# Kernel optimization log

Hardware: AMD Instinct MI355X
Metric: run time of the kernel (lower is better)

## Reference

```python
import jax, jax.numpy as jnp
import numpy as np

N_NODES, N_EDGES = 100000, 800000
F_NODE, F_EDGE, N_CLASSES = 128, 16, 10


def _lin(key, fan_in, fan_out, bias=True):
    k1, k2 = jax.random.split(key)
    W = jax.random.normal(k1, (fan_in, fan_out), jnp.float32) * 0.05
    if bias:
        b = jax.random.normal(k2, (fan_out,), jnp.float32) * 0.05
        return W, b
    return (W,)


def setup_inputs() -> dict:
    key = jax.random.key(0)
    ks = jax.random.split(key, 24)
    inp = {
        "x": jax.random.normal(ks[0], (N_NODES, F_NODE), jnp.float32),
        "edge_index": jax.random.randint(ks[1], (2, N_EDGES), 0, N_NODES, jnp.int64 if jax.config.jax_enable_x64 else jnp.int32),
        "edge_attr": jax.random.normal(ks[2], (N_EDGES, F_EDGE), jnp.float32),
    }
    dims = [(F_NODE, 128), (128, 128), (128, 256)]  # (in_channels, out_channels) per layer
    i = 3
    for li, (din, dout) in enumerate(dims, start=1):
        inp[f"Wq{li}"], inp[f"bq{li}"] = _lin(ks[i], din, dout); i += 1
        inp[f"Wk{li}"], inp[f"bk{li}"] = _lin(ks[i], din, dout); i += 1
        inp[f"Wv{li}"], inp[f"bv{li}"] = _lin(ks[i], din, dout); i += 1
        (inp[f"We{li}"],) = _lin(ks[i], F_EDGE, dout, bias=False); i += 1  # PyG lin_edge: bias=False
        inp[f"Ws{li}"], inp[f"bs{li}"] = _lin(ks[i], din, dout); i += 1  # root/skip weight
    inp["Wc"], inp["bc"] = _lin(ks[i], 256, N_CLASSES)
    return inp


def transformer_conv(x, src, dst, edge_attr, Wq, bq, Wk, bk, Wv, bv, We, Ws, bs):
    """PyG TransformerConv, heads=1, concat=True, root_weight=True."""
    N = x.shape[0]
    C = Wq.shape[1]
    q = x @ Wq + bq                      # [N, C]
    k = x @ Wk + bk                      # [N, C]
    v = x @ Wv + bv                      # [N, C]
    e = edge_attr @ We                   # [E, C] edge-conditioned term
    # per-edge attention logits: <q_i, k_j + e_ij> / sqrt(C)
    alpha = jnp.sum(q[dst] * (k[src] + e), axis=-1) / jnp.sqrt(jnp.float32(C))  # [E]
    # segment softmax over edges sharing a destination node
    m = jax.ops.segment_max(alpha, dst, num_segments=N)
    p = jnp.exp(alpha - m[dst])
    s = jax.ops.segment_sum(p, dst, num_segments=N)
    a = p / (s[dst] + 1e-16)
    # scatter-aggregate weighted messages (value_j + edge term)
    out = jax.ops.segment_sum(a[:, None] * (v[src] + e), dst, num_segments=N)  # [N, C]
    return out + x @ Ws + bs             # root/skip connection


def reference(x, edge_index, edge_attr,
              Wq1, bq1, Wk1, bk1, Wv1, bv1, We1, Ws1, bs1,
              Wq2, bq2, Wk2, bk2, Wv2, bv2, We2, Ws2, bs2,
              Wq3, bq3, Wk3, bk3, Wv3, bv3, We3, Ws3, bs3,
              Wc, bc):
    src, dst = edge_index[0], edge_index[1]
    h = transformer_conv(x, src, dst, edge_attr, Wq1, bq1, Wk1, bk1, Wv1, bv1, We1, Ws1, bs1)
    h = jax.nn.relu(h)  # dropout is identity in eval mode
    h = transformer_conv(h, src, dst, edge_attr, Wq2, bq2, Wk2, bk2, Wv2, bv2, We2, Ws2, bs2)
    h = jax.nn.relu(h)
    h = transformer_conv(h, src, dst, edge_attr, Wq3, bq3, Wk3, bk3, Wv3, bv3, We3, Ws3, bs3)
    return h @ Wc + bc                   # [N, num_classes]
```

## Files before the change

kernel.cpp:

```cpp
#include <hip/hip_runtime.h>
#include <math.h>


typedef unsigned int uint;
typedef unsigned short ushort;
typedef _Float16 f16x8 __attribute__((ext_vector_type(8)));
typedef _Float16 h16x2 __attribute__((ext_vector_type(2)));
typedef float f32x4 __attribute__((ext_vector_type(4)));
typedef float f32x2 __attribute__((ext_vector_type(2)));

__device__ __forceinline__ ushort f2h(float f) {
    return __builtin_bit_cast(ushort, (_Float16)f);
}
__device__ __forceinline__ float h2f(ushort h) {
    return (float)__builtin_bit_cast(_Float16, h);
}
__device__ __forceinline__ h16x2 bch2(uint u) { return __builtin_bit_cast(h16x2, u); }
__device__ __forceinline__ f32x2 cvt2(uint u) {
    h16x2 h = bch2(u);
    return (f32x2){(float)h.x, (float)h.y};
}

#if __has_builtin(__builtin_amdgcn_fdot2)
#define FDOT2(a, b, c) __builtin_amdgcn_fdot2((a), (b), (c), false)
#else
__device__ __forceinline__ float fdot2_sw(h16x2 a, h16x2 b, float c) {
    return fmaf((float)a.x, (float)b.x, fmaf((float)a.y, (float)b.y, c));
}
#define FDOT2(a, b, c) fdot2_sw((a), (b), (c))
#endif

__global__ void k_zero(uint* p, int n) {
    int i = blockIdx.x * 256 + threadIdx.x;
    if (i < n) p[i] = 0u;
}

__global__ void k_hist(const int* __restrict__ dst, uint* __restrict__ counts, int E, int N) {
    int e = blockIdx.x * 256 + threadIdx.x;
    if (e < E) {
        int d = dst[e];
        d = (d < 0) ? 0 : (d >= N ? N - 1 : d);
        atomicAdd(&counts[d], 1u);
    }
}

__global__ void k_scan1(const uint* __restrict__ counts, uint* __restrict__ bsum, int n) {
    __shared__ uint sm[256];
    int tid = threadIdx.x;
    int base = blockIdx.x * 1024 + tid * 4;
    uint s = 0;
#pragma unroll
    for (int j = 0; j < 4; ++j)
        if (base + j < n) s += counts[base + j];
    sm[tid] = s;
    __syncthreads();
    for (int d = 128; d > 0; d >>= 1) {
        if (tid < d) sm[tid] += sm[tid + d];
        __syncthreads();
    }
    if (tid == 0) bsum[blockIdx.x] = sm[0];
}

__global__ void k_scan2(uint* bsum, int nb) {
    if (threadIdx.x == 0 && blockIdx.x == 0) {
        uint run = 0;
        for (int i = 0; i < nb; ++i) { uint v = bsum[i]; bsum[i] = run; run += v; }
    }
}

__global__ void k_scan3(const uint* __restrict__ counts, const uint* __restrict__ bsum,
                        uint* __restrict__ row_ptr, int n, int E) {
    __shared__ uint sm[256];
    int tid = threadIdx.x;
    int base = blockIdx.x * 1024 + tid * 4;
    uint local[4];
    uint s = 0;
#pragma unroll
    for (int j = 0; j < 4; ++j) {
        local[j] = (base + j < n) ? counts[base + j] : 0u;
        s += local[j];
    }
    sm[tid] = s;
    __syncthreads();
    for (int d = 1; d < 256; d <<= 1) {
        uint v = (tid >= d) ? sm[tid - d] : 0u;
        __syncthreads();
        sm[tid] += v;
        __syncthreads();
    }
    uint run = sm[tid] - s + bsum[blockIdx.x];
#pragma unroll
    for (int j = 0; j < 4; ++j)
        if (base + j < n) { row_ptr[base + j] = run; run += local[j]; }
    if (blockIdx.x == 0 && tid == 0) row_ptr[n] = (uint)E;
}

__global__ void k_fill(const int* __restrict__ ei, const uint* __restrict__ row_ptr,
                       uint* __restrict__ cursor, int2* __restrict__ srcid, int E, int N) {
    int e = blockIdx.x * 256 + threadIdx.x;
    if (e >= E) return;
    int s = ei[e];
    int d = ei[E + e];
    s = (s < 0) ? 0 : (s >= N ? N - 1 : s);
    d = (d < 0) ? 0 : (d >= N ? N - 1 : d);
    uint idx = row_ptr[d] + atomicAdd(&cursor[d], 1u);
    srcid[idx] = make_int2(s, e);
}

__global__ void k_cvt(const float4* __restrict__ in, ushort4* __restrict__ outp, int n4) {
    int i = blockIdx.x * 256 + threadIdx.x;
    if (i >= n4) return;
    float4 v = in[i];
    ushort4 o;
    o.x = f2h(v.x); o.y = f2h(v.y); o.z = f2h(v.z); o.w = f2h(v.w);
    outp[i] = o;
}

__global__ void k_packg(const float* __restrict__ Wq, const float* __restrict__ bq,
                        const float* __restrict__ We, float* __restrict__ Wgf,
                        float* __restrict__ bgf, int C) {
    int id = blockIdx.x * 256 + threadIdx.x;
    if (id < 2048) {
        int k = id >> 4, f = id & 15;
        float s = 0.f;
        for (int c = 0; c < C; ++c) s = fmaf(Wq[k * C + c], We[f * C + c], s);
        Wgf[id] = s;
    } else if (id < 2064) {
        int f = id - 2048;
        float s = 0.f;
        for (int c = 0; c < C; ++c) s = fmaf(bq[c], We[f * C + c], s);
        bgf[f] = s;
    }
}

__global__ void k_packw(const float* __restrict__ Wq, const float* __restrict__ Wk,
                        const float* __restrict__ Wv, const float* __restrict__ Ws,
                        const float* __restrict__ Wgf, ushort* __restrict__ Bp, int C) {
    int nct = (4 * C + 16) >> 4;
    int total = 4 * nct * 512;
    int id = blockIdx.x * 256 + threadIdx.x;
    if (id >= total) return;
    int j = id & 7;
    int rest = id >> 3;
    int lane = rest & 63;
    rest >>= 6;
    int ct = rest % nct;
    int kt = rest / nct;
    int k = kt * 32 + ((lane >> 4) << 3) + j;
    int c = (ct << 4) + (lane & 15);
    float w;
    if (c < 4 * C) {
        int mat = c / C, cc = c % C;
        const float* W = (mat == 0) ? Wq : (mat == 1) ? Wk : (mat == 2) ? Wv : Ws;
        w = W[k * C + cc];
    } else {
        w = Wgf[k * 16 + (c - 4 * C)];
    }
    Bp[id] = f2h(w);
}

__global__ void k_bias(const float* __restrict__ bq, const float* __restrict__ bk,
                       const float* __restrict__ bv, const float* __restrict__ bs,
                       const float* __restrict__ bgf, float* __restrict__ outp, int C) {
    int c = blockIdx.x * 256 + threadIdx.x;
    if (c >= 4 * C + 16) return;
    float v;
    if (c < 4 * C) {
        int mat = c / C, cc = c % C;
        const float* b = (mat == 0) ? bq : (mat == 1) ? bk : (mat == 2) ? bv : bs;
        v = b[cc];
    } else {
        v = bgf[c - 4 * C];
    }
    outp[c] = v;
}

__global__ __launch_bounds__(256, 4) void k_gemm(const ushort* __restrict__ A,
                                                 const ushort* __restrict__ Bp,
                                                 const float* __restrict__ bias,
                                                 ushort* __restrict__ H,
                                                 ushort* __restrict__ S,
                                                 ushort* __restrict__ g,
                                                 int C, int mt_total) {
    constexpr int RT = 8;
    int fourC = 4 * C, threeC = 3 * C;
    int P = fourC + 16;
    int nct = P >> 4;
    int lane = threadIdx.x & 63;
    int wave = threadIdx.x >> 6;
    int quad = lane >> 4;
    int r = lane & 15;
    int c0 = (blockIdx.x << 8) + (wave << 6);
    int ct0 = c0 >> 4;
    if (ct0 >= nct) return;

    f16x8 bf[16];
#pragma unroll
    for (int kk = 0; kk < 4; ++kk)
#pragma unroll
        for (int i = 0; i < 4; ++i) {
            if (ct0 + i < nct)
                bf[kk * 4 + i] = *(const f16x8*)(Bp + ((size_t)((kk * nct + ct0 + i) << 6) + lane) * 8);
            else
                bf[kk * 4 + i] = __builtin_bit_cast(f16x8, (uint4){0u, 0u, 0u, 0u});
        }

    float bi4[4];
#pragma unroll
    for (int i = 0; i < 4; ++i) {
        int cc = c0 + (i << 4) + r;
        bi4[i] = (cc < P) ? bias[cc] : 0.f;
    }

    int mt0 = blockIdx.y * RT;
    int mt_end = mt0 + RT;
    if (mt_end > mt_total) mt_end = mt_total;

    for (int mt = mt0; mt < mt_end; ++mt) {
        int m0 = mt << 4;
        const ushort* arow = A + (size_t)(m0 + r) * 128 + (quad << 3);

        f32x4 acc[4];
#pragma unroll
        for (int i = 0; i < 4; ++i) acc[i] = (f32x4){0.f, 0.f, 0.f, 0.f};

#pragma unroll
        for (int kk = 0; kk < 4; ++kk) {
            f16x8 a = *(const f16x8*)(arow + kk * 32);
#pragma unroll
            for (int i = 0; i < 4; ++i)
                if (ct0 + i < nct)
                    acc[i] = __builtin_amdgcn_mfma_f32_16x16x32_f16(a, bf[kk * 4 + i], acc[i], 0, 0, 0);
        }

#pragma unroll
        for (int i = 0; i < 4; ++i) {
            int cc = c0 + (i << 4) + r;
            if (cc >= P) continue;
#pragma unroll
            for (int reg = 0; reg < 4; ++reg) {
                int rr = m0 + (quad << 2) + reg;
                ushort val = f2h(acc[i][reg] + bi4[i]);
                if (cc < threeC)      H[(size_t)rr * threeC + cc] = val;
                else if (cc < fourC)  S[(size_t)rr * C + (cc - threeC)] = val;
                else                  g[(size_t)rr * 16 + (cc - fourC)] = val;
            }
        }
    }
}

template <int C, int GSIZE>
__global__ __launch_bounds__(256, 6) void k_edge1(const ushort* __restrict__ H,
                                                  ushort* g,
                                                  const uint* __restrict__ row_ptr,
                                                  const int2* __restrict__ srcid,
                                                  const float* __restrict__ eattr,
                                                  ushort* __restrict__ ebuf,
                                                  float* __restrict__ lbuf, int N) {
    constexpr int VR = C / GSIZE;
    constexpr int TH = 3 * C;
    constexpr int GPB = 256 / GSIZE;
    const float scale = (C == 128) ? 0.08838834764831843f : 0.0625f;
    const float foldk = 16.0f / (float)GSIZE;

    int lane = threadIdx.x & (GSIZE - 1);
    int grp = threadIdx.x / GSIZE;
    int f = lane & 15;
    int node = blockIdx.x * GPB + grp;
    if (node >= N) return;
    int lvr = lane * VR;

    uint4 qv = *(const uint4*)(H + (size_t)node * TH + lvr);
    h16x2 q0 = bch2(qv.x), q1 = bch2(qv.y), q2 = bch2(qv.z), q3 = bch2(qv.w);
    float fg = foldk * h2f(g[(size_t)node * 16 + f]);
    uint beg = row_ptr[node], end = row_ptr[node + 1];

    float l = 0.f, w = 0.f;
    for (uint t = beg; t < end; t += 4) {
        uint t1 = (t + 1 < end) ? t + 1 : t;
        uint t2 = (t + 2 < end) ? t + 2 : t;
        uint t3 = (t + 3 < end) ? t + 3 : t;
        int2 se0 = srcid[t], se1 = srcid[t1], se2 = srcid[t2], se3 = srcid[t3];
        float at0 = eattr[(size_t)se0.y * 16 + f];
        float at1 = eattr[(size_t)se1.y * 16 + f];
        float at2 = eattr[(size_t)se2.y * 16 + f];
        float at3 = eattr[(size_t)se3.y * 16 + f];
        uint4 k0 = *(const uint4*)(H + (size_t)se0.x * TH + C + lvr);
        uint4 k1 = *(const uint4*)(H + (size_t)se1.x * TH + C + lvr);
        uint4 k2 = *(const uint4*)(H + (size_t)se2.x * TH + C + lvr);
        uint4 k3 = *(const uint4*)(H + (size_t)se3.x * TH + C + lvr);

        float p0 = at0 * fg, p1 = at1 * fg, p2 = at2 * fg, p3 = at3 * fg;
        p0 = FDOT2(q0, bch2(k0.x), p0); p0 = FDOT2(q1, bch2(k0.y), p0);
        p0 = FDOT2(q2, bch2(k0.z), p0); p0 = FDOT2(q3, bch2(k0.w), p0);
        p1 = FDOT2(q0, bch2(k1.x), p1); p1 = FDOT2(q1, bch2(k1.y), p1);
        p1 = FDOT2(q2, bch2(k1.z), p1); p1 = FDOT2(q3, bch2(k1.w), p1);
        p2 = FDOT2(q0, bch2(k2.x), p2); p2 = FDOT2(q1, bch2(k2.y), p2);
        p2 = FDOT2(q2, bch2(k2.z), p2); p2 = FDOT2(q3, bch2(k2.w), p2);
        p3 = FDOT2(q0, bch2(k3.x), p3); p3 = FDOT2(q1, bch2(k3.y), p3);
        p3 = FDOT2(q2, bch2(k3.z), p3); p3 = FDOT2(q3, bch2(k3.w), p3);

        p0 += __shfl_xor(p0, 1); p1 += __shfl_xor(p1, 1);
        p2 += __shfl_xor(p2, 1); p3 += __shfl_xor(p3, 1);
        p0 += __shfl_xor(p0, 2); p1 += __shfl_xor(p1, 2);
        p2 += __shfl_xor(p2, 2); p3 += __shfl_xor(p3, 2);
        p0 += __shfl_xor(p0, 4); p1 += __shfl_xor(p1, 4);
        p2 += __shfl_xor(p2, 4); p3 += __shfl_xor(p3, 4);
        p0 += __shfl_xor(p0, 8); p1 += __shfl_xor(p1, 8);
        p2 += __shfl_xor(p2, 8); p3 += __shfl_xor(p3, 8);
        if (GSIZE == 32) {
            p0 += __shfl_xor(p0, 16); p1 += __shfl_xor(p1, 16);
            p2 += __shfl_xor(p2, 16); p3 += __shfl_xor(p3, 16);
        }
        float e0 = __expf(p0 * scale);
        float e1 = (t + 1 < end) ? __expf(p1 * scale) : 0.f;
        float e2 = (t + 2 < end) ? __expf(p2 * scale) : 0.f;
        float e3 = (t + 3 < end) ? __expf(p3 * scale) : 0.f;
        l += (e0 + e1) + (e2 + e3);
        w = fmaf(e0, at0, w); w = fmaf(e1, at1, w);
        w = fmaf(e2, at2, w); w = fmaf(e3, at3, w);
        if (lane < 4) {
            uint tj = t + lane;
            if (tj < end) {
                float ee = (lane == 0) ? e0 : (lane == 1) ? e1 : (lane == 2) ? e2 : e3;
                ebuf[tj] = f2h(ee);
            }
        }
    }
    if (lane < 16) g[(size_t)node * 16 + lane] = f2h(w);
    if (lane == 0) lbuf[node] = l;
}

template <int C, int GSIZE, bool RELU>
__global__ __launch_bounds__(256, 6) void k_edge2(const ushort* __restrict__ H,
                                                  ushort* __restrict__ S,
                                                  const uint* __restrict__ row_ptr,
                                                  const int2* __restrict__ srcid,
                                                  const ushort* __restrict__ ebuf,
                                                  const ushort* __restrict__ wbuf,
                                                  const float* __restrict__ lbuf,
                                                  const float* __restrict__ We, int N) {
    constexpr int VR = C / GSIZE;
    constexpr int TH = 3 * C;
    constexpr int GPB = 256 / GSIZE;
    __shared__ float swex[GPB][17];

    int lane = threadIdx.x & (GSIZE - 1);
    int grp = threadIdx.x / GSIZE;
    int node = blockIdx.x * GPB + grp;
    if (node >= N) return;
    int lvr = lane * VR;
    uint beg = row_ptr[node], end = row_ptr[node + 1];

    ushort* srow = S + (size_t)node * C + lvr;
    uint4 skv = *(const uint4*)srow;
    if (lane < 16) swex[grp][lane] = h2f(wbuf[(size_t)node * 16 + lane]);
    float l = lbuf[node];

    f32x2 acc[4];
#pragma unroll
    for (int j = 0; j < 4; ++j) acc[j] = (f32x2){0.f, 0.f};

    for (uint t = beg; t < end; t += 4) {
        uint t1 = (t + 1 < end) ? t + 1 : t;
        uint t2 = (t + 2 < end) ? t + 2 : t;
        uint t3 = (t + 3 < end) ? t + 3 : t;
        int s0 = srcid[t].x, s1 = srcid[t1].x, s2 = srcid[t2].x, s3 = srcid[t3].x;
        float e0 = h2f(ebuf[t]);
        float e1 = (t + 1 < end) ? h2f(ebuf[t1]) : 0.f;
        float e2 = (t + 2 < end) ? h2f(ebuf[t2]) : 0.f;
        float e3 = (t + 3 < end) ? h2f(ebuf[t3]) : 0.f;
        uint4 v0 = *(const uint4*)(H + (size_t)s0 * TH + 2 * C + lvr);
        uint4 v1 = *(const uint4*)(H + (size_t)s1 * TH + 2 * C + lvr);
        uint4 v2 = *(const uint4*)(H + (size_t)s2 * TH + 2 * C + lvr);
        uint4 v3 = *(const uint4*)(H + (size_t)s3 * TH + 2 * C + lvr);
        f32x2 eb;
        eb = (f32x2){e0, e0};
        acc[0] = __builtin_elementwise_fma(cvt2(v0.x), eb, acc[0]);
        acc[1] = __builtin_elementwise_fma(cvt2(v0.y), eb, acc[1]);
        acc[2] = __builtin_elementwise_fma(cvt2(v0.z), eb, acc[2]);
        acc[3] = __builtin_elementwise_fma(cvt2(v0.w), eb, acc[3]);
        eb = (f32x2){e1, e1};
        acc[0] = __builtin_elementwise_fma(cvt2(v1.x), eb, acc[0]);
        acc[1] = __builtin_elementwise_fma(cvt2(v1.y), eb, acc[1]);
        acc[2] = __builtin_elementwise_fma(cvt2(v1.z), eb, acc[2]);
        acc[3] = __builtin_elementwise_fma(cvt2(v1.w), eb, acc[3]);
        eb = (f32x2){e2, e2};
        acc[0] = __builtin_elementwise_fma(cvt2(v2.x), eb, acc[0]);
        acc[1] = __builtin_elementwise_fma(cvt2(v2.y), eb, acc[1]);
        acc[2] = __builtin_elementwise_fma(cvt2(v2.z), eb, acc[2]);
        acc[3] = __builtin_elementwise_fma(cvt2(v2.w), eb, acc[3]);
        eb = (f32x2){e3, e3};
        acc[0] = __builtin_elementwise_fma(cvt2(v3.x), eb, acc[0]);
        acc[1] = __builtin_elementwise_fma(cvt2(v3.y), eb, acc[1]);
        acc[2] = __builtin_elementwise_fma(cvt2(v3.z), eb, acc[2]);
        acc[3] = __builtin_elementwise_fma(cvt2(v3.w), eb, acc[3]);
    }

    float inv = 1.f / (l + 1e-16f);
    f32x2 ew[4];
#pragma unroll
    for (int j = 0; j < 4; ++j) ew[j] = (f32x2){0.f, 0.f};
#pragma unroll
    for (int f2i = 0; f2i < 16; ++f2i) {
        float wfs = swex[grp][f2i];
        f32x2 wf = (f32x2){wfs, wfs};
        const f32x4* wrow = (const f32x4*)(We + f2i * C + lvr);
        f32x4 c0 = wrow[0], c1 = wrow[1];
        ew[0] = __builtin_elementwise_fma(c0.lo, wf, ew[0]);
        ew[1] = __builtin_elementwise_fma(c0.hi, wf, ew[1]);
        ew[2] = __builtin_elementwise_fma(c1.lo, wf, ew[2]);
        ew[3] = __builtin_elementwise_fma(c1.hi, wf, ew[3]);
    }
    const uint* sp = (const uint*)&skv;
    uint4 ov;
    uint* op = (uint*)&ov;
#pragma unroll
    for (int hh = 0; hh < 4; ++hh) {
        f32x2 sk = cvt2(sp[hh]);
        float o0 = (acc[hh].x + ew[hh].x) * inv + sk.x;
        float o1 = (acc[hh].y + ew[hh].y) * inv + sk.y;
        if (RELU) { o0 = fmaxf(o0, 0.f); o1 = fmaxf(o1, 0.f); }
        op[hh] = (uint)f2h(o0) | ((uint)f2h(o1) << 16);
    }
    *(uint4*)srow = ov;
}

__global__ void k_cls(const ushort* __restrict__ h, const float* __restrict__ Wc,
                      const float* __restrict__ bc, float* __restrict__ outp, int N) {
    int t = blockIdx.x * 256 + threadIdx.x;
    int node = t >> 4;
    int c = t & 15;
    if (node >= N || c >= 10) return;
    const ushort* hr = h + (size_t)node * 256;
    float acc = 0.f;
#pragma unroll 4
    for (int k4 = 0; k4 < 64; ++k4) {
        uint2 u = *(const uint2*)(hr + k4 * 4);
        f32x2 a01 = cvt2(u.x);
        f32x2 a23 = cvt2(u.y);
        int kb = k4 * 4;
        acc = fmaf(a01.x, Wc[(kb + 0) * 10 + c], acc);
        acc = fmaf(a01.y, Wc[(kb + 1) * 10 + c], acc);
        acc = fmaf(a23.x, Wc[(kb + 2) * 10 + c], acc);
        acc = fmaf(a23.y, Wc[(kb + 3) * 10 + c], acc);
    }
    outp[node * 10 + c] = acc + bc[c];
}

extern "C" void kernel_launch(void* const* d_in, const int* in_sizes, int n_in,
                              void* d_out, int out_size, void* d_ws, size_t ws_size,
                              hipStream_t stream) {
    const float* x = (const float*)d_in[0];
    const int* ei = (const int*)d_in[1];
    const float* eattr = (const float*)d_in[2];
    const int N = in_sizes[0] / 128;
    const int E = in_sizes[1] / 2;

    const float* Wq[3], *bq[3], *Wk[3], *bk[3], *Wv[3], *bv[3], *We[3], *Ws[3], *bs[3];
    for (int li = 0; li < 3; ++li) {
        int base = 3 + li * 9;
        Wq[li] = (const float*)d_in[base + 0];
        bq[li] = (const float*)d_in[base + 1];
        Wk[li] = (const float*)d_in[base + 2];
        bk[li] = (const float*)d_in[base + 3];
        Wv[li] = (const float*)d_in[base + 4];
        bv[li] = (const float*)d_in[base + 5];
        We[li] = (const float*)d_in[base + 6];
        Ws[li] = (const float*)d_in[base + 7];
        bs[li] = (const float*)d_in[base + 8];
    }
    const float* Wc = (const float*)d_in[30];
    const float* bc = (const float*)d_in[31];

    size_t off = 0;
    char* base = (char*)d_ws;
    auto alloc = [&](size_t bytes) -> void* {
        void* p = base + off;
        off = (off + bytes + 255) & ~(size_t)255;
        return p;
    };
    ushort* SA = (ushort*)alloc((size_t)N * 256 * 2);
    ushort* SB = (ushort*)alloc((size_t)N * 128 * 2);
    ushort* H  = (ushort*)alloc((size_t)N * 768 * 2);
    ushort* gbuf = (ushort*)alloc((size_t)N * 16 * 2);
    ushort* Bp = (ushort*)alloc(140000 * 2);
    float* biasc = (float*)alloc(1040 * 4);
    float* Wgf = (float*)alloc(2048 * 4);
    float* bgf = (float*)alloc(16 * 4);
    uint* row_ptr = (uint*)alloc((size_t)(N + 1) * 4);
    uint* counts = (uint*)alloc((size_t)N * 4);
    uint* cursor = (uint*)alloc((size_t)N * 4);
    uint* bsum = (uint*)alloc(1024 * 4);
    int2* srcid = (int2*)alloc((size_t)E * 8);
    ushort* ebuf = (ushort*)alloc((size_t)E * 2);

    ushort* xb = SB;
    float* lbuf = (float*)counts;

    int nb = (N + 1023) / 1024;

    k_zero<<<(N + 255) / 256, 256, 0, stream>>>(counts, N);
    k_zero<<<(N + 255) / 256, 256, 0, stream>>>(cursor, N);
    k_hist<<<(E + 255) / 256, 256, 0, stream>>>(ei + E, counts, E, N);
    k_scan1<<<nb, 256, 0, stream>>>(counts, bsum, N);
    k_scan2<<<1, 64, 0, stream>>>(bsum, nb);
    k_scan3<<<nb, 256, 0, stream>>>(counts, bsum, row_ptr, N, E);
    k_fill<<<(E + 255) / 256, 256, 0, stream>>>(ei, row_ptr, cursor, srcid, E, N);

    int n4 = N * 128 / 4;
    k_cvt<<<(n4 + 255) / 256, 256, 0, stream>>>((const float4*)x, (ushort4*)xb, n4);

    int mt_total = N / 16;
    for (int li = 0; li < 3; ++li) {
        int C = (li == 2) ? 256 : 128;
        int P = 4 * C + 16;
        int packTotal = 4 * (P >> 4) * 512;
        const ushort* A = (li == 0) ? xb : (li == 1) ? SA : SB;
        ushort* Sout = (li == 1) ? SB : SA;

        k_packg<<<9, 256, 0, stream>>>(Wq[li], bq[li], We[li], Wgf, bgf, C);
        k_packw<<<(packTotal + 255) / 256, 256, 0, stream>>>(Wq[li], Wk[li], Wv[li], Ws[li], Wgf, Bp, C);
        k_bias<<<(P + 255) / 256, 256, 0, stream>>>(bq[li], bk[li], bv[li], bs[li], bgf, biasc, C);
        k_gemm<<<dim3((P + 255) / 256, (mt_total + 7) / 8), 256, 0, stream>>>(A, Bp, biasc, H, Sout, gbuf, C, mt_total);
        if (li == 2) {
            k_edge1<256, 32><<<(N * 32 + 255) / 256, 256, 0, stream>>>(H, gbuf, row_ptr, srcid, eattr, ebuf, lbuf, N);
            k_edge2<256, 32, false><<<(N * 32 + 255) / 256, 256, 0, stream>>>(H, Sout, row_ptr, srcid, ebuf, gbuf, lbuf, We[li], N);
        } else {
            k_edge1<128, 16><<<(N * 16 + 255) / 256, 256, 0, stream>>>(H, gbuf, row_ptr, srcid, eattr, ebuf, lbuf, N);
            k_edge2<128, 16, true><<<(N * 16 + 255) / 256, 256, 0, stream>>>(H, Sout, row_ptr, srcid, ebuf, gbuf, lbuf, We[li], N);
        }
    }

    k_cls<<<(N * 16 + 255) / 256, 256, 0, stream>>>(SA, Wc, bc, (float*)d_out, N);
}
```

Measured before the change: 985.8 us.

## Sort nodes by in-degree to balance edge kernel workloads

Builds a permutation of nodes bucketed by in-degree (capped at 63) using a histogram, a serial scan and an atomic fill, and has both edge kernels process nodes in that order. Groups in a wavefront then walk similar-length edge lists, which cuts divergence and idle lanes in the per-node loops. In exchange it adds four small kernels and an extra indirection. It also loses the locality of contiguous node ids for the H, S and g row accesses, and bucket order within a degree is nondeterministic.

```diff
diff --git a/kernel.cpp b/kernel.cpp
--- a/kernel.cpp
+++ b/kernel.cpp
@@ -105,6 +105,33 @@
     d = (d < 0) ? 0 : (d >= N ? N - 1 : d);
     uint idx = row_ptr[d] + atomicAdd(&cursor[d], 1u);
     srcid[idx] = make_int2(s, e);
+}
+
+__global__ void k_dhist(const uint* __restrict__ row_ptr, uint* __restrict__ dcnt, int N) {
+    int i = blockIdx.x * 256 + threadIdx.x;
+    if (i < N) {
+        uint d = row_ptr[i + 1] - row_ptr[i];
+        if (d > 63u) d = 63u;
+        atomicAdd(&dcnt[d], 1u);
+    }
+}
+
+__global__ void k_dscan(uint* dcnt) {
+    if (threadIdx.x == 0 && blockIdx.x == 0) {
+        uint run = 0;
+        for (int i = 0; i < 64; ++i) { uint v = dcnt[i]; dcnt[i] = run; run += v; }
+    }
+}
+
+__global__ void k_dfill(const uint* __restrict__ row_ptr, uint* __restrict__ dcur,
+                        uint* __restrict__ perm, int N) {
+    int i = blockIdx.x * 256 + threadIdx.x;
+    if (i < N) {
+        uint d = row_ptr[i + 1] - row_ptr[i];
+        if (d > 63u) d = 63u;
+        uint idx = atomicAdd(&dcur[d], 1u);
+        perm[idx] = (uint)i;
+    }
 }
 
 __global__ void k_cvt(const float4* __restrict__ in, ushort4* __restrict__ outp, int n4) {
@@ -255,6 +282,7 @@
                                                   const uint* __restrict__ row_ptr,
                                                   const int2* __restrict__ srcid,
                                                   const float* __restrict__ eattr,
+                                                  const uint* __restrict__ perm,
                                                   ushort* __restrict__ ebuf,
                                                   float* __restrict__ lbuf, int N) {
     constexpr int VR = C / GSIZE;
@@ -266,8 +294,9 @@
     int lane = threadIdx.x & (GSIZE - 1);
     int grp = threadIdx.x / GSIZE;
     int f = lane & 15;
-    int node = blockIdx.x * GPB + grp;
-    if (node >= N) return;
+    int slot = blockIdx.x * GPB + grp;
+    if (slot >= N) return;
+    int node = (int)perm[slot];
     int lvr = lane * VR;
 
     uint4 qv = *(const uint4*)(H + (size_t)node * TH + lvr);
@@ -339,6 +368,7 @@
                                                   const ushort* __restrict__ ebuf,
                                                   const ushort* __restrict__ wbuf,
                                                   const float* __restrict__ lbuf,
+                                                  const uint* __restrict__ perm,
                                                   const float* __restrict__ We, int N) {
     constexpr int VR = C / GSIZE;
     constexpr int TH = 3 * C;
@@ -347,8 +377,9 @@
 
     int lane = threadIdx.x & (GSIZE - 1);
     int grp = threadIdx.x / GSIZE;
-    int node = blockIdx.x * GPB + grp;
-    if (node >= N) return;
+    int slot = blockIdx.x * GPB + grp;
+    if (slot >= N) return;
+    int node = (int)perm[slot];
     int lvr = lane * VR;
     uint beg = row_ptr[node], end = row_ptr[node + 1];
 
@@ -494,6 +525,8 @@
     uint* bsum = (uint*)alloc(1024 * 4);
     int2* srcid = (int2*)alloc((size_t)E * 8);
     ushort* ebuf = (ushort*)alloc((size_t)E * 2);
+    uint* perm = (uint*)alloc((size_t)N * 4);
+    uint* dcnt = (uint*)alloc(64 * 4);
 
     ushort* xb = SB;
     float* lbuf = (float*)counts;
@@ -508,6 +541,11 @@
     k_scan3<<<nb, 256, 0, stream>>>(counts, bsum, row_ptr, N, E);
     k_fill<<<(E + 255) / 256, 256, 0, stream>>>(ei, row_ptr, cursor, srcid, E, N);
 
+    k_zero<<<1, 64, 0, stream>>>(dcnt, 64);
+    k_dhist<<<(N + 255) / 256, 256, 0, stream>>>(row_ptr, dcnt, N);
+    k_dscan<<<1, 64, 0, stream>>>(dcnt);
+    k_dfill<<<(N + 255) / 256, 256, 0, stream>>>(row_ptr, dcnt, perm, N);
+
     int n4 = N * 128 / 4;
     k_cvt<<<(n4 + 255) / 256, 256, 0, stream>>>((const float4*)x, (ushort4*)xb, n4);
 
@@ -524,11 +562,11 @@
         k_bias<<<(P + 255) / 256, 256, 0, stream>>>(bq[li], bk[li], bv[li], bs[li], bgf, biasc, C);
         k_gemm<<<dim3((P + 255) / 256, (mt_total + 7) / 8), 256, 0, stream>>>(A, Bp, biasc, H, Sout, gbuf, C, mt_total);
         if (li == 2) {
-            k_edge1<256, 32><<<(N * 32 + 255) / 256, 256, 0, stream>>>(H, gbuf, row_ptr, srcid, eattr, ebuf, lbuf, N);
-            k_edge2<256, 32, false><<<(N * 32 + 255) / 256, 256, 0, stream>>>(H, Sout, row_ptr, srcid, ebuf, gbuf, lbuf, We[li], N);
+            k_edge1<256, 32><<<(N * 32 + 255) / 256, 256, 0, stream>>>(H, gbuf, row_ptr, srcid, eattr, perm, ebuf, lbuf, N);
+            k_edge2<256, 32, false><<<(N * 32 + 255) / 256, 256, 0, stream>>>(H, Sout, row_ptr, srcid, ebuf, gbuf, lbuf, perm, We[li], N);
         } else {
-            k_edge1<128, 16><<<(N * 16 + 255) / 256, 256, 0, stream>>>(H, gbuf, row_ptr, srcid, eattr, ebuf, lbuf, N);
-            k_edge2<128, 16, true><<<(N * 16 + 255) / 256, 256, 0, stream>>>(H, Sout, row_ptr, srcid, ebuf, gbuf, lbuf, We[li], N);
+            k_edge1<128, 16><<<(N * 16 + 255) / 256, 256, 0, stream>>>(H, gbuf, row_ptr, srcid, eattr, perm, ebuf, lbuf, N);
+            k_edge2<128, 16, true><<<(N * 16 + 255) / 256, 256, 0, stream>>>(H, Sout, row_ptr, srcid, ebuf, gbuf, lbuf, perm, We[li], N);
         }
     }
 
```

Result: slower. 1.703 ms (+72.7%).
